# Performance work log

Measured on AMD Instinct MI355X. Metric: run time of the kernel, lower is better.

The kernel has to match this reference:

```python
import jax, jax.numpy as jnp
import numpy as np

B = 8192; L = 68; NPG = L + 1; N = B * NPG
IN = 4; HID = 64; OUT = 7; NL = 8
BN_EPS = 1e-5


def setup_inputs() -> dict:
    key = jax.random.key(0)
    ks = jax.random.split(key, 12)
    # graph topology (same for every graph): ring among L landmarks + master node (idx L)
    # connected to every landmark; directed edges both ways (PyG-style edge_index).
    ring = np.stack([np.arange(L), (np.arange(L) + 1) % L])            # [2, L]
    mast = np.stack([np.arange(L), np.full(L, L)])                     # [2, L]
    und = np.concatenate([ring, mast], axis=1)                         # [2, 2L]
    e = np.concatenate([und, und[::-1]], axis=1)                       # [2, 4L]
    offs = (np.arange(B) * NPG)[:, None, None]
    edge_index = (e[None] + offs).transpose(1, 0, 2).reshape(2, -1)    # [2, B*4L]
    s = 1.0 / np.sqrt(HID)
    return {
        "x": jax.random.normal(ks[0], (N, IN), jnp.float32),
        "edge_index": jnp.asarray(edge_index, jnp.int32),
        "batch": jnp.repeat(jnp.arange(B, dtype=jnp.int32), NPG),
        "master_mask": jnp.tile(jnp.arange(NPG) == L, B),
        "conv_first_W": jax.random.normal(ks[1], (IN, HID), jnp.float32) * 0.5,
        "conv_first_b": jnp.zeros((HID,), jnp.float32),
        "conv_mid_W": jax.random.normal(ks[2], (NL - 2, HID, HID), jnp.float32) * s,
        "conv_mid_b": jnp.zeros((NL - 2, HID), jnp.float32),
        "conv_last_W": jax.random.normal(ks[3], (HID, HID), jnp.float32) * s,
        "conv_last_b": jnp.zeros((HID,), jnp.float32),
        "bn_gamma": jnp.ones((NL - 1, HID), jnp.float32),
        "bn_beta": jnp.zeros((NL - 1, HID), jnp.float32),
        "bn_mean": jax.random.normal(ks[4], (NL - 1, HID), jnp.float32) * 0.1,
        "bn_var": jax.random.uniform(ks[5], (NL - 1, HID), jnp.float32) * 0.5 + 0.5,
        "att_W1": jax.random.normal(ks[6], (HID, HID), jnp.float32) * s,
        "att_b1": jnp.zeros((HID,), jnp.float32),
        "att_W2": jax.random.normal(ks[7], (HID, 1), jnp.float32) * s,
        "att_b2": jnp.zeros((1,), jnp.float32),
        "fc1_W": jax.random.normal(ks[8], (3 * HID, HID), jnp.float32) / np.sqrt(3 * HID),
        "fc1_b": jnp.zeros((HID,), jnp.float32),
        "fc2_W": jax.random.normal(ks[9], (HID, OUT), jnp.float32) * s,
        "fc2_b": jnp.zeros((OUT,), jnp.float32),
    }


def reference(x, edge_index, batch, master_mask,
              conv_first_W, conv_first_b, conv_mid_W, conv_mid_b,
              conv_last_W, conv_last_b, bn_gamma, bn_beta, bn_mean, bn_var,
              att_W1, att_b1, att_W2, att_b2, fc1_W, fc1_b, fc2_W, fc2_b):
    n = x.shape[0]
    src, dst = edge_index[0], edge_index[1]
    # GCN symmetric normalization with self-loops: deg_i = 1 + in-degree
    deg = 1.0 + jax.ops.segment_sum(jnp.ones_like(src, x.dtype), dst, num_segments=n)
    dis = jax.lax.rsqrt(deg)
    enorm = (dis[src] * dis[dst])[:, None]                 # [E,1]
    self_norm = (1.0 / deg)[:, None]                       # [N,1] self-loop coeff

    def gcn(h, W, b):
        h = h @ W                                          # [N,HID]
        agg = jax.ops.segment_sum(h[src] * enorm, dst, num_segments=n)
        return agg + h * self_norm + b

    def bn(h, i):  # eval-mode BatchNorm1d
        return bn_gamma[i] * (h - bn_mean[i]) * jax.lax.rsqrt(bn_var[i] + BN_EPS) + bn_beta[i]

    h = bn(jax.nn.relu(gcn(x, conv_first_W, conv_first_b)), 0)
    for i in range(NL - 2):  # residual GCN blocks
        h = bn(jax.nn.relu(gcn(h, conv_mid_W[i], conv_mid_b[i])), i + 1) + h
    h = jax.nn.relu(gcn(h, conv_last_W, conv_last_b))

    mfl = master_mask.astype(h.dtype)                      # [N]
    mcnt = jax.ops.segment_sum(mfl, batch, num_segments=B)
    master = jax.ops.segment_sum(h * mfl[:, None], batch, num_segments=B) / mcnt[:, None]
    att = jax.nn.sigmoid(jax.nn.relu(master @ att_W1 + att_b1) @ att_W2 + att_b2)
    master = master * att

    rfl = 1.0 - mfl
    rcnt = jax.ops.segment_sum(rfl, batch, num_segments=B)
    x_mean = jax.ops.segment_sum(h * rfl[:, None], batch, num_segments=B) / rcnt[:, None]
    h_masked = jnp.where(master_mask[:, None], -jnp.inf, h)
    x_max = jax.ops.segment_max(h_masked, batch, num_segments=B)

    g = jnp.concatenate([x_mean, x_max, master], axis=1)   # [B, 3*HID]
    return jax.nn.relu(g @ fc1_W + fc1_b) @ fc2_W + fc2_b  # [B, OUT]
```

## Files before the change

kernel.cpp:

```cpp
#include <hip/hip_runtime.h>

typedef float f32x4 __attribute__((ext_vector_type(4)));
typedef short short8 __attribute__((ext_vector_type(8)));
typedef unsigned int u32;
typedef unsigned short u16;

#define CLL 0.25f
#define CML 0.06019292654288460f
#define SELFM 0.014492753623188406f

__device__ __forceinline__ u16 f2bf(float x) {
  u32 b = __float_as_uint(x);
  return (u16)((b + 0x7FFFu + ((b >> 16) & 1u)) >> 16);
}
__device__ __forceinline__ u32 cvtpk(float a, float b) {
  u32 r;
  asm("v_cvt_pk_bf16_f32 %0, %1, %2" : "=v"(r) : "v"(a), "v"(b));
  return r;
}

__global__ void prep(const float* __restrict__ midW, const float* __restrict__ lastW,
                     const float* __restrict__ bng, const float* __restrict__ bnb,
                     const float* __restrict__ bnm, const float* __restrict__ bnv,
                     u16* __restrict__ frag, float* __restrict__ bns) {
  const int t0 = blockIdx.x * blockDim.x + threadIdx.x;
  for (int u = t0; u < 7 * 4 * 2 * 64; u += gridDim.x * blockDim.x) {
    const int lane = u & 63;
    const int t = u >> 6;
    const int ks = t & 1;
    const int nt = (t >> 1) & 3;
    const int l = t >> 3;
    const float* W = (l < 6) ? (midW + l * 4096) : lastW;
    const int col = nt * 16 + (lane & 15);
    const int kb = ks * 32 + (lane >> 4) * 8;
    u16* dst = frag + (size_t)u * 8;
#pragma unroll
    for (int j = 0; j < 8; ++j) dst[j] = f2bf(W[(kb + j) * 64 + col]);
  }
  for (int u = t0; u < 7 * 64; u += gridDim.x * blockDim.x) {
    const int l = u >> 6, f = u & 63;
    const float sc = (float)((double)bng[l * 64 + f] / sqrt((double)bnv[l * 64 + f] + 1e-5));
    bns[l * 128 + f] = sc;
    bns[l * 128 + 64 + f] = bnb[l * 64 + f] - bnm[l * 64 + f] * sc;
  }
}

#define SUM4(V) ((V)[0] + (V)[1] + (V)[2] + (V)[3])
#define MAX4(V) fmaxf(fmaxf((V)[0], (V)[1]), fmaxf((V)[2], (V)[3]))

#define STEP2(MT, TA, TPA, TNA, TB, TPB, TNB, HA, HB, RESID)           \
  {                                                                    \
    const float spA_ = (qg == 3) ? TPA[3] : TA[3];                     \
    const float spB_ = (qg == 3) ? TPB[3] : TB[3];                     \
    const u32 pvP_ = (u32)__shfl((int)cvtpk(spA_, spB_), (lane + 48) & 63, 64); \
    const float snA_ = (qg == 0) ? TNA[0] : TA[0];                     \
    const float snB_ = (qg == 0) ? TNB[0] : TB[0];                     \
    const u32 nvP_ = (u32)__shfl((int)cvtpk(snA_, snB_), (lane + 16) & 63, 64); \
    const float pvA_ = __uint_as_float(pvP_ << 16);                    \
    const float pvB_ = __uint_as_float(pvP_ & 0xffff0000u);            \
    const float nvA_ = __uint_as_float(nvP_ << 16);                    \
    const float nvB_ = __uint_as_float(nvP_ & 0xffff0000u);            \
    const float ta0A_ = ((MT) == 0 && qg == 0) ? tA4[3] : pvA_;        \
    const float ta0B_ = ((MT) == 0 && qg == 0) ? tB4[3] : pvB_;        \
    const float tb3A_ = ((MT) == 4 && qg == 0) ? tA0[0] : nvA_;        \
    const float tb3B_ = ((MT) == 4 && qg == 0) ? tB0[0] : nvB_;        \
    float oA0 = fmaf(CLL, ta0A_ + TA[0] + TA[1], cmtA_);               \
    float oA1 = fmaf(CLL, TA[0] + TA[1] + TA[2], cmtA_);               \
    float oA2 = fmaf(CLL, TA[1] + TA[2] + TA[3], cmtA_);               \
    float oA3 = fmaf(CLL, TA[2] + TA[3] + tb3A_, cmtA_);               \
    float oB0 = fmaf(CLL, ta0B_ + TB[0] + TB[1], cmtB_);               \
    float oB1 = fmaf(CLL, TB[0] + TB[1] + TB[2], cmtB_);               \
    float oB2 = fmaf(CLL, TB[1] + TB[2] + TB[3], cmtB_);               \
    float oB3 = fmaf(CLL, TB[2] + TB[3] + tb3B_, cmtB_);               \
    oA0 = fmaf(fmaxf(oA0, 0.f), scA_, shA_);                           \
    oA1 = fmaf(fmaxf(oA1, 0.f), scA_, shA_);                           \
    oA2 = fmaf(fmaxf(oA2, 0.f), scA_, shA_);                           \
    oA3 = fmaf(fmaxf(oA3, 0.f), scA_, shA_);                           \
    oB0 = fmaf(fmaxf(oB0, 0.f), scB_, shB_);                           \
    oB1 = fmaf(fmaxf(oB1, 0.f), scB_, shB_);                           \
    oB2 = fmaf(fmaxf(oB2, 0.f), scB_, shB_);                           \
    oB3 = fmaf(fmaxf(oB3, 0.f), scB_, shB_);                           \
    if (RESID) {                                                       \
      oA0 += HA[0]; oA1 += HA[1]; oA2 += HA[2]; oA3 += HA[3];          \
      oB0 += HB[0]; oB1 += HB[1]; oB2 += HB[2]; oB3 += HB[3];          \
    }                                                                  \
    HA[0] = oA0; HA[1] = oA1; HA[2] = oA2; HA[3] = oA3;                \
    HB[0] = oB0; HB[1] = oB1; HB[2] = oB2; HB[3] = oB3;                \
  }

#define WPAIR2(HW, MT, H, CQ)                                          \
  {                                                                    \
    const u32 pa = cvtpk(H[0], H[1]);                                  \
    const u32 pb = cvtpk(H[2], H[3]);                                  \
    (HW)[(16 * (MT) + 4 * qg + 0) * 64 + (CQ)] = (u16)pa;              \
    (HW)[(16 * (MT) + 4 * qg + 1) * 64 + ((CQ) ^ 8)] = (u16)(pa >> 16);\
    (HW)[(16 * (MT) + 4 * qg + 2) * 64 + ((CQ) ^ 16)] = (u16)pb;       \
    (HW)[(16 * (MT) + 4 * qg + 3) * 64 + ((CQ) ^ 24)] = (u16)(pb >> 16); \
  }

#define EPILOG2(RESID, WRITE, HBW, BA, BB, SCA, SHA, SCB, SHB)         \
  {                                                                    \
    float SA_ = SUM4(tA0) + SUM4(tA1) + SUM4(tA2) + SUM4(tA3) + SUM4(tA4); \
    float SB_ = SUM4(tB0) + SUM4(tB1) + SUM4(tB2) + SUM4(tB3) + SUM4(tB4); \
    if (qg == 1) { SA_ -= tA4[0]; SB_ -= tB4[0]; }                     \
    SA_ += __shfl_xor(SA_, 16, 64);                                    \
    SA_ += __shfl_xor(SA_, 32, 64);                                    \
    SB_ += __shfl_xor(SB_, 16, 64);                                    \
    SB_ += __shfl_xor(SB_, 32, 64);                                    \
    const u32 pk_ = (u32)__shfl((int)cvtpk(tA4[0], tB4[0]), 16 + p15, 64); \
    const float scA_ = (SCA), shA_ = (SHA), scB_ = (SCB), shB_ = (SHB);\
    const float cmtA_ = fmaf(CML, __uint_as_float(pk_ << 16), (BA));   \
    const float cmtB_ = fmaf(CML, __uint_as_float(pk_ & 0xffff0000u), (BB)); \
    float mvA_ = 0.f, mvB_ = 0.f;                                      \
    if (qg == 1) {                                                     \
      mvA_ = fmaf(fmaxf(fmaf(CML, SA_, fmaf(SELFM, tA4[0], (BA))), 0.f), scA_, shA_); \
      mvB_ = fmaf(fmaxf(fmaf(CML, SB_, fmaf(SELFM, tB4[0], (BB))), 0.f), scB_, shB_); \
      if (RESID) { mvA_ += hA4[0]; mvB_ += hB4[0]; }                   \
    }                                                                  \
    STEP2(0, tA0, tA4, tA1, tB0, tB4, tB1, hA0, hB0, RESID)            \
    STEP2(1, tA1, tA0, tA2, tB1, tB0, tB2, hA1, hB1, RESID)            \
    STEP2(2, tA2, tA1, tA3, tB2, tB1, tB3, hA2, hB2, RESID)            \
    STEP2(3, tA3, tA2, tA4, tB3, tB2, tB4, hA3, hB3, RESID)            \
    STEP2(4, tA4, tA3, tA0, tB4, tB3, tB0, hA4, hB4, RESID)            \
    if (qg == 1) { hA4[0] = mvA_; hB4[0] = mvB_; }                     \
    if (WRITE) {                                                       \
      u16* hw_ = (HBW);                                                \
      WPAIR2(hw_, 0, hA0, cqA) WPAIR2(hw_, 0, hB0, cqB)                \
      WPAIR2(hw_, 1, hA1, cqA) WPAIR2(hw_, 1, hB1, cqB)                \
      WPAIR2(hw_, 2, hA2, cqA) WPAIR2(hw_, 2, hB2, cqB)                \
      WPAIR2(hw_, 3, hA3, cqA) WPAIR2(hw_, 3, hB3, cqB)                \
      if (qg == 0) { WPAIR2(hw_, 4, hA4, cqA) WPAIR2(hw_, 4, hB4, cqB) } \
      else if (qg == 1) {                                              \
        hw_[68 * 64 + (cA ^ 32)] = (u16)cvtpk(mvA_, mvA_);             \
        hw_[68 * 64 + (cB ^ 32)] = (u16)cvtpk(mvB_, mvB_);             \
      }                                                                \
    }                                                                  \
  }

#define MM(A, B, C) __builtin_amdgcn_mfma_f32_16x16x32_bf16(A, B, C, 0, 0, 0)

#define MP3(HR, MT, TA, TB)                                            \
  {                                                                    \
    const short8 a0 = *(const short8*)&(HR)[(MT) * 1024 + ra0];        \
    const short8 a1 = *(const short8*)&(HR)[(MT) * 1024 + ra1];        \
    f32x4 accA = z4, accB = z4;                                        \
    accA = MM(a0, bA0, accA); accA = MM(a1, bA1, accA);                \
    accB = MM(a0, bB0, accB); accB = MM(a1, bB1, accB);                \
    TA = accA; TB = accB;                                              \
  }

__launch_bounds__(128)
__global__ void gcn_fused(
    const float* __restrict__ x,
    const float* __restrict__ cfW, const float* __restrict__ cfb,
    const float* __restrict__ cmb, const float* __restrict__ clb,
    const float* __restrict__ aW1, const float* __restrict__ ab1,
    const float* __restrict__ aW2, const float* __restrict__ ab2,
    const float* __restrict__ f1W, const float* __restrict__ f1b,
    const float* __restrict__ f2W, const float* __restrict__ f2b,
    const u16* __restrict__ frag, const float* __restrict__ bns,
    float* __restrict__ out) {
  __shared__ u16 hb[2][80 * 64];
  __shared__ float xl4[80 * 4];
  __shared__ float mrow[64];
  __shared__ float gv[192];
  __shared__ float part[128];

  const int tid = threadIdx.x;
  const int g = blockIdx.x;
  const int lane = tid & 63;
  const int w = tid >> 6;
  const int p15 = lane & 15;
  const int qg = lane >> 4;
  const int cA = w * 32 + p15;
  const int cB = cA + 16;
  const f32x4 z4 = {0.f, 0.f, 0.f, 0.f};

  const int rsw = (p15 & 7) << 3;
  const int ra0 = (p15 * 64 + qg * 8) ^ rsw;
  const int ra1 = (p15 * 64 + 32 + qg * 8) ^ rsw;
  const int cqA = cA ^ ((qg & 1) << 5);
  const int cqB = cqA ^ 16;

  const u16* f0p = frag + (((size_t)(2 * w) * 2) * 64 + lane) * 8;
  const u16* f1p = frag + (((size_t)(2 * w + 1) * 2) * 64 + lane) * 8;
  short8 bA0 = *(const short8*)f0p;
  short8 bA1 = *(const short8*)(f0p + 512);
  short8 bB0 = *(const short8*)f1p;
  short8 bB1 = *(const short8*)(f1p + 512);

  {
    u32* hz = (u32*)hb;
#pragma unroll
    for (int it = 0; it < 3; ++it) {
      const int i = tid + it * 128;
      if (i < 352) {
        hz[2208 + i] = 0u;
        hz[2560 + 2208 + i] = 0u;
      }
    }
  }
  if (tid < 69)
    *(f32x4*)&xl4[tid * 4] = *(const f32x4*)&x[((size_t)g * 69 + tid) * 4];
  else if (tid < 80)
    *(f32x4*)&xl4[tid * 4] = z4;

  f32x4 tA0, tA1, tA2, tA3, tA4, tB0, tB1, tB2, tB3, tB4;
  f32x4 hA0, hA1, hA2, hA3, hA4, hB0, hB1, hB2, hB3, hB4;

  __syncthreads();

  {
    const float wA0 = cfW[cA], wA1 = cfW[64 + cA], wA2 = cfW[128 + cA], wA3 = cfW[192 + cA];
    const float wB0 = cfW[cB], wB1 = cfW[64 + cB], wB2 = cfW[128 + cB], wB3 = cfW[192 + cB];
#define L0T(MT, TA, TB)                                                \
    { _Pragma("unroll") for (int r = 0; r < 4; ++r) {                  \
        const f32x4 xv = *(const f32x4*)&xl4[(16 * (MT) + 4 * qg + r) * 4]; \
        TA[r] = fmaf(xv[0], wA0, fmaf(xv[1], wA1, fmaf(xv[2], wA2, xv[3] * wA3))); \
        TB[r] = fmaf(xv[0], wB0, fmaf(xv[1], wB1, fmaf(xv[2], wB2, xv[3] * wB3))); } }
    L0T(0, tA0, tB0) L0T(1, tA1, tB1) L0T(2, tA2, tB2) L0T(3, tA3, tB3) L0T(4, tA4, tB4)
#undef L0T
  }
  EPILOG2(false, true, &hb[0][0], cfb[cA], cfb[cB], bns[cA], bns[64 + cA],
          bns[cB], bns[64 + cB])
  __syncthreads();

#pragma unroll 1
  for (int l = 1; l <= 6; ++l) {
    const u16* fA = frag + ((((size_t)l * 4 + 2 * w) * 2) * 64 + lane) * 8;
    const u16* fB = frag + ((((size_t)l * 4 + 2 * w + 1) * 2) * 64 + lane) * 8;
    const short8 nA0 = *(const short8*)fA;
    const short8 nA1 = *(const short8*)(fA + 512);
    const short8 nB0 = *(const short8*)fB;
    const short8 nB1 = *(const short8*)(fB + 512);
    const float biasA = cmb[(l - 1) * 64 + cA];
    const float biasB = cmb[(l - 1) * 64 + cB];
    const float lscA = bns[l * 128 + cA], lshA = bns[l * 128 + 64 + cA];
    const float lscB = bns[l * 128 + cB], lshB = bns[l * 128 + 64 + cB];
    const u16* hr = &hb[(l + 1) & 1][0];
    MP3(hr, 0, tA0, tB0) MP3(hr, 1, tA1, tB1) MP3(hr, 2, tA2, tB2)
    MP3(hr, 3, tA3, tB3) MP3(hr, 4, tA4, tB4)
    bA0 = nA0; bA1 = nA1; bB0 = nB0; bB1 = nB1;
    EPILOG2(true, true, &hb[l & 1][0], biasA, biasB, lscA, lshA, lscB, lshB)
    __syncthreads();
  }

  {
    const u16* hr = &hb[0][0];
    MP3(hr, 0, tA0, tB0) MP3(hr, 1, tA1, tB1) MP3(hr, 2, tA2, tB2)
    MP3(hr, 3, tA3, tB3) MP3(hr, 4, tA4, tB4)
    EPILOG2(false, false, (u16*)nullptr, clb[cA], clb[cB], 1.f, 0.f, 1.f, 0.f)
  }

  {
    float sA = SUM4(hA0) + SUM4(hA1) + SUM4(hA2) + SUM4(hA3);
    float sB = SUM4(hB0) + SUM4(hB1) + SUM4(hB2) + SUM4(hB3);
    float mA = fmaxf(fmaxf(MAX4(hA0), MAX4(hA1)), fmaxf(MAX4(hA2), MAX4(hA3)));
    float mB = fmaxf(fmaxf(MAX4(hB0), MAX4(hB1)), fmaxf(MAX4(hB2), MAX4(hB3)));
    if (qg == 0) {
      sA += SUM4(hA4); mA = fmaxf(mA, MAX4(hA4));
      sB += SUM4(hB4); mB = fmaxf(mB, MAX4(hB4));
    }
    sA += __shfl_xor(sA, 16, 64); sA += __shfl_xor(sA, 32, 64);
    sB += __shfl_xor(sB, 16, 64); sB += __shfl_xor(sB, 32, 64);
    mA = fmaxf(mA, __shfl_xor(mA, 16, 64)); mA = fmaxf(mA, __shfl_xor(mA, 32, 64));
    mB = fmaxf(mB, __shfl_xor(mB, 16, 64)); mB = fmaxf(mB, __shfl_xor(mB, 32, 64));
    if (qg == 0) {
      gv[cA] = sA * (1.f / 68.f);
      gv[64 + cA] = mA;
      gv[cB] = sB * (1.f / 68.f);
      gv[64 + cB] = mB;
    }
    if (qg == 1) { mrow[cA] = hA4[0]; mrow[cB] = hB4[0]; }
  }
  __syncthreads();

  {
    const int f = tid & 63;
    const int kh = tid >> 6;
    float z = 0.f;
#pragma unroll
    for (int k = 0; k < 32; ++k)
      z = fmaf(mrow[kh * 32 + k], aW1[(kh * 32 + k) * 64 + f], z);
    part[tid] = z;
  }
  __syncthreads();
  if (tid < 64) {
    float z = part[tid] + part[64 + tid] + ab1[tid];
    z = fmaxf(z, 0.f);
    float pr = z * aW2[tid];
#pragma unroll
    for (int off = 32; off > 0; off >>= 1) pr += __shfl_xor(pr, off, 64);
    const float att = 1.f / (1.f + expf(-(pr + ab2[0])));
    gv[128 + tid] = mrow[tid] * att;
  }
  __syncthreads();

  {
    const int f = tid & 63;
    const int ih = tid >> 6;
    float a = 0.f;
#pragma unroll
    for (int i = 0; i < 96; ++i)
      a = fmaf(gv[ih * 96 + i], f1W[(ih * 96 + i) * 64 + f], a);
    part[tid] = a;
  }
  __syncthreads();
  if (tid < 64) {
    float a = part[tid] + part[64 + tid] + f1b[tid];
    const float y = fmaxf(a, 0.f);
    float po[7];
#pragma unroll
    for (int o = 0; o < 7; ++o) po[o] = y * f2W[tid * 7 + o];
#pragma unroll
    for (int o = 0; o < 7; ++o)
#pragma unroll
      for (int off = 32; off > 0; off >>= 1) po[o] += __shfl_xor(po[o], off, 64);
    if (tid == 0) {
#pragma unroll
      for (int o = 0; o < 7; ++o) out[(size_t)g * 7 + o] = po[o] + f2b[o];
    }
  }
}

extern "C" void kernel_launch(void* const* d_in, const int* in_sizes, int n_in,
                              void* d_out, int out_size, void* d_ws, size_t ws_size,
                              hipStream_t stream) {
  (void)in_sizes; (void)n_in; (void)ws_size;
  const float* x   = (const float*)d_in[0];
  const float* cfW = (const float*)d_in[4];
  const float* cfb = (const float*)d_in[5];
  const float* cmW = (const float*)d_in[6];
  const float* cmb = (const float*)d_in[7];
  const float* clW = (const float*)d_in[8];
  const float* clb = (const float*)d_in[9];
  const float* bng = (const float*)d_in[10];
  const float* bnb = (const float*)d_in[11];
  const float* bnm = (const float*)d_in[12];
  const float* bnv = (const float*)d_in[13];
  const float* aW1 = (const float*)d_in[14];
  const float* ab1 = (const float*)d_in[15];
  const float* aW2 = (const float*)d_in[16];
  const float* ab2 = (const float*)d_in[17];
  const float* f1W = (const float*)d_in[18];
  const float* f1b = (const float*)d_in[19];
  const float* f2W = (const float*)d_in[20];
  const float* f2b = (const float*)d_in[21];

  u16* frag = (u16*)d_ws;
  float* bns = (float*)((char*)d_ws + 57344);
  const int ngraphs = out_size / 7;

  prep<<<dim3(16), dim3(256), 0, stream>>>(cmW, clW, bng, bnb, bnm, bnv, frag, bns);
  gcn_fused<<<dim3(ngraphs), dim3(128), 0, stream>>>(
      x, cfW, cfb, cmb, clb, aW1, ab1, aW2, ab2, f1W, f1b, f2W, f2b,
      frag, bns, (float*)d_out);
}
```

Before: 157.0 us.

## Map one graph per wavefront, packing four graphs per block without barriers

Previously two wavefronts shared each graph, each computing 32 of the 64 feature columns, and they synchronized with __syncthreads after every layer. Now one wavefront handles a whole graph: it computes all 64 columns in two halves per layer. It reads the A operands into registers first, so the single LDS activation buffer can be overwritten in place. The attention and fc1 head loops run inside the same wave, so block-level barriers and the partial-sum scratch buffer go away. The cost is roughly double the live register state per thread and a serial second half of each layer. That can lower occupancy or cause spills in exchange for less synchronization and fewer blocks.

```diff
diff --git a/kernel.cpp b/kernel.cpp
--- a/kernel.cpp
+++ b/kernel.cpp
@@ -47,6 +47,7 @@
 
 #define SUM4(V) ((V)[0] + (V)[1] + (V)[2] + (V)[3])
 #define MAX4(V) fmaxf(fmaxf((V)[0], (V)[1]), fmaxf((V)[2], (V)[3]))
+#define MM(A, B, C) __builtin_amdgcn_mfma_f32_16x16x32_bf16(A, B, C, 0, 0, 0)
 
 #define STEP2(MT, TA, TPA, TNA, TB, TPB, TNB, HA, HB, RESID)           \
   {                                                                    \
@@ -80,7 +81,7 @@
     oB1 = fmaf(fmaxf(oB1, 0.f), scB_, shB_);                           \
     oB2 = fmaf(fmaxf(oB2, 0.f), scB_, shB_);                           \
     oB3 = fmaf(fmaxf(oB3, 0.f), scB_, shB_);                           \
-    if (RESID) {                                                       \
+    if (RESID) {                                                      \
       oA0 += HA[0]; oA1 += HA[1]; oA2 += HA[2]; oA3 += HA[3];          \
       oB0 += HB[0]; oB1 += HB[1]; oB2 += HB[2]; oB3 += HB[3];          \
     }                                                                  \
@@ -98,15 +99,14 @@
     (HW)[(16 * (MT) + 4 * qg + 3) * 64 + ((CQ) ^ 24)] = (u16)(pb >> 16); \
   }
 
-#define EPILOG2(RESID, WRITE, HBW, BA, BB, SCA, SHA, SCB, SHB)         \
+#define EPILOG2(HA0, HA1, HA2, HA3, HA4, HB0, HB1, HB2, HB3, HB4,      \
+                CQA_, CQB_, CA_, CB_, RESID, WRITE, BA, BB, SCA, SHA, SCB, SHB) \
   {                                                                    \
     float SA_ = SUM4(tA0) + SUM4(tA1) + SUM4(tA2) + SUM4(tA3) + SUM4(tA4); \
     float SB_ = SUM4(tB0) + SUM4(tB1) + SUM4(tB2) + SUM4(tB3) + SUM4(tB4); \
     if (qg == 1) { SA_ -= tA4[0]; SB_ -= tB4[0]; }                     \
-    SA_ += __shfl_xor(SA_, 16, 64);                                    \
-    SA_ += __shfl_xor(SA_, 32, 64);                                    \
-    SB_ += __shfl_xor(SB_, 16, 64);                                    \
-    SB_ += __shfl_xor(SB_, 32, 64);                                    \
+    SA_ += __shfl_xor(SA_, 16, 64); SA_ += __shfl_xor(SA_, 32, 64);    \
+    SB_ += __shfl_xor(SB_, 16, 64); SB_ += __shfl_xor(SB_, 32, 64);    \
     const u32 pk_ = (u32)__shfl((int)cvtpk(tA4[0], tB4[0]), 16 + p15, 64); \
     const float scA_ = (SCA), shA_ = (SHA), scB_ = (SCB), shB_ = (SHB);\
     const float cmtA_ = fmaf(CML, __uint_as_float(pk_ << 16), (BA));   \
@@ -115,41 +115,67 @@
     if (qg == 1) {                                                     \
       mvA_ = fmaf(fmaxf(fmaf(CML, SA_, fmaf(SELFM, tA4[0], (BA))), 0.f), scA_, shA_); \
       mvB_ = fmaf(fmaxf(fmaf(CML, SB_, fmaf(SELFM, tB4[0], (BB))), 0.f), scB_, shB_); \
-      if (RESID) { mvA_ += hA4[0]; mvB_ += hB4[0]; }                   \
+      if (RESID) { mvA_ += HA4[0]; mvB_ += HB4[0]; }                   \
     }                                                                  \
-    STEP2(0, tA0, tA4, tA1, tB0, tB4, tB1, hA0, hB0, RESID)            \
-    STEP2(1, tA1, tA0, tA2, tB1, tB0, tB2, hA1, hB1, RESID)            \
-    STEP2(2, tA2, tA1, tA3, tB2, tB1, tB3, hA2, hB2, RESID)            \
-    STEP2(3, tA3, tA2, tA4, tB3, tB2, tB4, hA3, hB3, RESID)            \
-    STEP2(4, tA4, tA3, tA0, tB4, tB3, tB0, hA4, hB4, RESID)            \
-    if (qg == 1) { hA4[0] = mvA_; hB4[0] = mvB_; }                     \
+    STEP2(0, tA0, tA4, tA1, tB0, tB4, tB1, HA0, HB0, RESID)            \
+    STEP2(1, tA1, tA0, tA2, tB1, tB0, tB2, HA1, HB1, RESID)            \
+    STEP2(2, tA2, tA1, tA3, tB2, tB1, tB3, HA2, HB2, RESID)            \
+    STEP2(3, tA3, tA2, tA4, tB3, tB2, tB4, HA3, HB3, RESID)            \
+    STEP2(4, tA4, tA3, tA0, tB4, tB3, tB0, HA4, HB4, RESID)            \
+    if (qg == 1) { HA4[0] = mvA_; HB4[0] = mvB_; }                     \
     if (WRITE) {                                                       \
-      u16* hw_ = (HBW);                                                \
-      WPAIR2(hw_, 0, hA0, cqA) WPAIR2(hw_, 0, hB0, cqB)                \
-      WPAIR2(hw_, 1, hA1, cqA) WPAIR2(hw_, 1, hB1, cqB)                \
-      WPAIR2(hw_, 2, hA2, cqA) WPAIR2(hw_, 2, hB2, cqB)                \
-      WPAIR2(hw_, 3, hA3, cqA) WPAIR2(hw_, 3, hB3, cqB)                \
-      if (qg == 0) { WPAIR2(hw_, 4, hA4, cqA) WPAIR2(hw_, 4, hB4, cqB) } \
+      WPAIR2(hb, 0, HA0, CQA_) WPAIR2(hb, 0, HB0, CQB_)                \
+      WPAIR2(hb, 1, HA1, CQA_) WPAIR2(hb, 1, HB1, CQB_)                \
+      WPAIR2(hb, 2, HA2, CQA_) WPAIR2(hb, 2, HB2, CQB_)                \
+      WPAIR2(hb, 3, HA3, CQA_) WPAIR2(hb, 3, HB3, CQB_)                \
+      if (qg == 0) { WPAIR2(hb, 4, HA4, CQA_) WPAIR2(hb, 4, HB4, CQB_) } \
       else if (qg == 1) {                                              \
-        hw_[68 * 64 + (cA ^ 32)] = (u16)cvtpk(mvA_, mvA_);             \
-        hw_[68 * 64 + (cB ^ 32)] = (u16)cvtpk(mvB_, mvB_);             \
+        hb[68 * 64 + ((CA_) ^ 32)] = (u16)cvtpk(mvA_, mvA_);           \
+        hb[68 * 64 + ((CB_) ^ 32)] = (u16)cvtpk(mvB_, mvB_);           \
       }                                                                \
     }                                                                  \
   }
 
-#define MM(A, B, C) __builtin_amdgcn_mfma_f32_16x16x32_bf16(A, B, C, 0, 0, 0)
-
-#define MP3(HR, MT, TA, TB)                                            \
-  {                                                                    \
-    const short8 a0 = *(const short8*)&(HR)[(MT) * 1024 + ra0];        \
-    const short8 a1 = *(const short8*)&(HR)[(MT) * 1024 + ra1];        \
-    f32x4 accA = z4, accB = z4;                                        \
-    accA = MM(a0, bA0, accA); accA = MM(a1, bA1, accA);                \
-    accB = MM(a0, bB0, accB); accB = MM(a1, bB1, accB);                \
-    TA = accA; TB = accB;                                              \
-  }
-
-__launch_bounds__(128)
+#define RD_A()                                                         \
+  qa0 = *(const short8*)&hb[0 * 1024 + ra0]; qb0 = *(const short8*)&hb[0 * 1024 + ra1]; \
+  qa1 = *(const short8*)&hb[1 * 1024 + ra0]; qb1 = *(const short8*)&hb[1 * 1024 + ra1]; \
+  qa2 = *(const short8*)&hb[2 * 1024 + ra0]; qb2 = *(const short8*)&hb[2 * 1024 + ra1]; \
+  qa3 = *(const short8*)&hb[3 * 1024 + ra0]; qb3 = *(const short8*)&hb[3 * 1024 + ra1]; \
+  qa4 = *(const short8*)&hb[4 * 1024 + ra0]; qb4 = *(const short8*)&hb[4 * 1024 + ra1];
+
+#define LDB(LF, NT0, NT1)                                              \
+  {                                                                    \
+    const u16* fa_ = frag + (((size_t)(LF) * 4 + (NT0)) * 2 * 64 + lane) * 8; \
+    const u16* fb_ = frag + (((size_t)(LF) * 4 + (NT1)) * 2 * 64 + lane) * 8; \
+    bA0 = *(const short8*)fa_; bA1 = *(const short8*)(fa_ + 512);      \
+    bB0 = *(const short8*)fb_; bB1 = *(const short8*)(fb_ + 512);      \
+  }
+
+#define MPX(QA, QB, TA, TB)                                            \
+  {                                                                    \
+    f32x4 uA_ = z4, uB_ = z4;                                          \
+    uA_ = MM(QA, bA0, uA_); uA_ = MM(QB, bA1, uA_);                    \
+    uB_ = MM(QA, bB0, uB_); uB_ = MM(QB, bB1, uB_);                    \
+    TA = uA_; TB = uB_;                                                \
+  }
+
+#define MFMA_PAIR() \
+  MPX(qa0, qb0, tA0, tB0) MPX(qa1, qb1, tA1, tB1) MPX(qa2, qb2, tA2, tB2) \
+  MPX(qa3, qb3, tA3, tB3) MPX(qa4, qb4, tA4, tB4)
+
+#define RDOUT(H0, H1, H2, H3, H4, C_)                                  \
+  {                                                                    \
+    float s_ = SUM4(H0) + SUM4(H1) + SUM4(H2) + SUM4(H3);              \
+    float m_ = fmaxf(fmaxf(MAX4(H0), MAX4(H1)), fmaxf(MAX4(H2), MAX4(H3))); \
+    if (qg == 0) { s_ += SUM4(H4); m_ = fmaxf(m_, MAX4(H4)); }         \
+    s_ += __shfl_xor(s_, 16, 64); s_ += __shfl_xor(s_, 32, 64);        \
+    m_ = fmaxf(m_, __shfl_xor(m_, 16, 64));                            \
+    m_ = fmaxf(m_, __shfl_xor(m_, 32, 64));                            \
+    if (qg == 0) { gv[C_] = s_ * (1.f / 68.f); gv[64 + C_] = m_; }     \
+    if (qg == 1) mrow[C_] = H4[0];                                     \
+  }
+
+__launch_bounds__(256)
 __global__ void gcn_fused(
     const float* __restrict__ x,
     const float* __restrict__ cfW, const float* __restrict__ cfb,
@@ -159,21 +185,25 @@
     const float* __restrict__ f1W, const float* __restrict__ f1b,
     const float* __restrict__ f2W, const float* __restrict__ f2b,
     const u16* __restrict__ frag, const float* __restrict__ bns,
-    float* __restrict__ out) {
-  __shared__ u16 hb[2][80 * 64];
-  __shared__ float xl4[80 * 4];
-  __shared__ float mrow[64];
-  __shared__ float gv[192];
-  __shared__ float part[128];
-
-  const int tid = threadIdx.x;
-  const int g = blockIdx.x;
-  const int lane = tid & 63;
-  const int w = tid >> 6;
+    float* __restrict__ out, int ngraphs) {
+  __shared__ u16 hbAll[4][80 * 64];
+  __shared__ float xlAll[4][80 * 4];
+  __shared__ float mrowAll[4][64];
+  __shared__ float gvAll[4][192];
+
+  const int lane = threadIdx.x & 63;
+  const int w = threadIdx.x >> 6;
+  const int g = blockIdx.x * 4 + w;
+  if (g >= ngraphs) return;
+
+  u16* hb = hbAll[w];
+  float* xl4 = xlAll[w];
+  float* mrow = mrowAll[w];
+  float* gv = gvAll[w];
+
   const int p15 = lane & 15;
   const int qg = lane >> 4;
-  const int cA = w * 32 + p15;
-  const int cB = cA + 16;
+  const int cA = p15, cB = p15 + 16, cC = p15 + 32, cD = p15 + 48;
   const f32x4 z4 = {0.f, 0.f, 0.f, 0.f};
 
   const int rsw = (p15 & 7) << 3;
@@ -181,142 +211,109 @@
   const int ra1 = (p15 * 64 + 32 + qg * 8) ^ rsw;
   const int cqA = cA ^ ((qg & 1) << 5);
   const int cqB = cqA ^ 16;
-
-  const u16* f0p = frag + (((size_t)(2 * w) * 2) * 64 + lane) * 8;
-  const u16* f1p = frag + (((size_t)(2 * w + 1) * 2) * 64 + lane) * 8;
-  short8 bA0 = *(const short8*)f0p;
-  short8 bA1 = *(const short8*)(f0p + 512);
-  short8 bB0 = *(const short8*)f1p;
-  short8 bB1 = *(const short8*)(f1p + 512);
-
-  {
-    u32* hz = (u32*)hb;
-#pragma unroll
-    for (int it = 0; it < 3; ++it) {
-      const int i = tid + it * 128;
-      if (i < 352) {
-        hz[2208 + i] = 0u;
-        hz[2560 + 2208 + i] = 0u;
-      }
-    }
-  }
-  if (tid < 69)
-    *(f32x4*)&xl4[tid * 4] = *(const f32x4*)&x[((size_t)g * 69 + tid) * 4];
-  else if (tid < 80)
-    *(f32x4*)&xl4[tid * 4] = z4;
+  const int cqC = cqA ^ 32;
+  const int cqD = cqA ^ 48;
+
+  for (int i = lane; i < 352; i += 64) ((u32*)hb)[2208 + i] = 0u;
+  *(f32x4*)&xl4[lane * 4] = *(const f32x4*)&x[((size_t)g * 69 + lane) * 4];
+  if (lane < 5)
+    *(f32x4*)&xl4[(64 + lane) * 4] = *(const f32x4*)&x[((size_t)g * 69 + 64 + lane) * 4];
+  else if (lane < 16)
+    *(f32x4*)&xl4[(64 + lane) * 4] = z4;
 
   f32x4 tA0, tA1, tA2, tA3, tA4, tB0, tB1, tB2, tB3, tB4;
   f32x4 hA0, hA1, hA2, hA3, hA4, hB0, hB1, hB2, hB3, hB4;
-
-  __syncthreads();
-
-  {
-    const float wA0 = cfW[cA], wA1 = cfW[64 + cA], wA2 = cfW[128 + cA], wA3 = cfW[192 + cA];
-    const float wB0 = cfW[cB], wB1 = cfW[64 + cB], wB2 = cfW[128 + cB], wB3 = cfW[192 + cB];
-#define L0T(MT, TA, TB)                                                \
-    { _Pragma("unroll") for (int r = 0; r < 4; ++r) {                  \
-        const f32x4 xv = *(const f32x4*)&xl4[(16 * (MT) + 4 * qg + r) * 4]; \
-        TA[r] = fmaf(xv[0], wA0, fmaf(xv[1], wA1, fmaf(xv[2], wA2, xv[3] * wA3))); \
-        TB[r] = fmaf(xv[0], wB0, fmaf(xv[1], wB1, fmaf(xv[2], wB2, xv[3] * wB3))); } }
-    L0T(0, tA0, tB0) L0T(1, tA1, tB1) L0T(2, tA2, tB2) L0T(3, tA3, tB3) L0T(4, tA4, tB4)
+  f32x4 hC0, hC1, hC2, hC3, hC4, hD0, hD1, hD2, hD3, hD4;
+  short8 qa0, qa1, qa2, qa3, qa4, qb0, qb1, qb2, qb3, qb4;
+  short8 bA0, bA1, bB0, bB1;
+
+#define L0T(MT, TA, TB, W0A, W1A, W2A, W3A, W0B, W1B, W2B, W3B)        \
+  { _Pragma("unroll") for (int r = 0; r < 4; ++r) {                    \
+      const f32x4 xv = *(const f32x4*)&xl4[(16 * (MT) + 4 * qg + r) * 4]; \
+      TA[r] = fmaf(xv[0], W0A, fmaf(xv[1], W1A, fmaf(xv[2], W2A, xv[3] * W3A))); \
+      TB[r] = fmaf(xv[0], W0B, fmaf(xv[1], W1B, fmaf(xv[2], W2B, xv[3] * W3B))); } }
+  {
+    const float a0 = cfW[cA], a1 = cfW[64 + cA], a2 = cfW[128 + cA], a3 = cfW[192 + cA];
+    const float b0 = cfW[cB], b1 = cfW[64 + cB], b2 = cfW[128 + cB], b3 = cfW[192 + cB];
+    L0T(0, tA0, tB0, a0, a1, a2, a3, b0, b1, b2, b3)
+    L0T(1, tA1, tB1, a0, a1, a2, a3, b0, b1, b2, b3)
+    L0T(2, tA2, tB2, a0, a1, a2, a3, b0, b1, b2, b3)
+    L0T(3, tA3, tB3, a0, a1, a2, a3, b0, b1, b2, b3)
+    L0T(4, tA4, tB4, a0, a1, a2, a3, b0, b1, b2, b3)
+    EPILOG2(hA0, hA1, hA2, hA3, hA4, hB0, hB1, hB2, hB3, hB4, cqA, cqB, cA, cB,
+            false, true, cfb[cA], cfb[cB], bns[cA], bns[64 + cA], bns[cB], bns[64 + cB])
+  }
+  {
+    const float a0 = cfW[cC], a1 = cfW[64 + cC], a2 = cfW[128 + cC], a3 = cfW[192 + cC];
+    const float b0 = cfW[cD], b1 = cfW[64 + cD], b2 = cfW[128 + cD], b3 = cfW[192 + cD];
+    L0T(0, tA0, tB0, a0, a1, a2, a3, b0, b1, b2, b3)
+    L0T(1, tA1, tB1, a0, a1, a2, a3, b0, b1, b2, b3)
+    L0T(2, tA2, tB2, a0, a1, a2, a3, b0, b1, b2, b3)
+    L0T(3, tA3, tB3, a0, a1, a2, a3, b0, b1, b2, b3)
+    L0T(4, tA4, tB4, a0, a1, a2, a3, b0, b1, b2, b3)
+    EPILOG2(hC0, hC1, hC2, hC3, hC4, hD0, hD1, hD2, hD3, hD4, cqC, cqD, cC, cD,
+            false, true, cfb[cC], cfb[cD], bns[cC], bns[64 + cC], bns[cD], bns[64 + cD])
+  }
 #undef L0T
-  }
-  EPILOG2(false, true, &hb[0][0], cfb[cA], cfb[cB], bns[cA], bns[64 + cA],
-          bns[cB], bns[64 + cB])
-  __syncthreads();
 
 #pragma unroll 1
   for (int l = 1; l <= 6; ++l) {
-    const u16* fA = frag + ((((size_t)l * 4 + 2 * w) * 2) * 64 + lane) * 8;
-    const u16* fB = frag + ((((size_t)l * 4 + 2 * w + 1) * 2) * 64 + lane) * 8;
-    const short8 nA0 = *(const short8*)fA;
-    const short8 nA1 = *(const short8*)(fA + 512);
-    const short8 nB0 = *(const short8*)fB;
-    const short8 nB1 = *(const short8*)(fB + 512);
-    const float biasA = cmb[(l - 1) * 64 + cA];
-    const float biasB = cmb[(l - 1) * 64 + cB];
-    const float lscA = bns[l * 128 + cA], lshA = bns[l * 128 + 64 + cA];
-    const float lscB = bns[l * 128 + cB], lshB = bns[l * 128 + 64 + cB];
-    const u16* hr = &hb[(l + 1) & 1][0];
-    MP3(hr, 0, tA0, tB0) MP3(hr, 1, tA1, tB1) MP3(hr, 2, tA2, tB2)
-    MP3(hr, 3, tA3, tB3) MP3(hr, 4, tA4, tB4)
-    bA0 = nA0; bA1 = nA1; bB0 = nB0; bB1 = nB1;
-    EPILOG2(true, true, &hb[l & 1][0], biasA, biasB, lscA, lshA, lscB, lshB)
-    __syncthreads();
-  }
-
-  {
-    const u16* hr = &hb[0][0];
-    MP3(hr, 0, tA0, tB0) MP3(hr, 1, tA1, tB1) MP3(hr, 2, tA2, tB2)
-    MP3(hr, 3, tA3, tB3) MP3(hr, 4, tA4, tB4)
-    EPILOG2(false, false, (u16*)nullptr, clb[cA], clb[cB], 1.f, 0.f, 1.f, 0.f)
-  }
-
-  {
-    float sA = SUM4(hA0) + SUM4(hA1) + SUM4(hA2) + SUM4(hA3);
-    float sB = SUM4(hB0) + SUM4(hB1) + SUM4(hB2) + SUM4(hB3);
-    float mA = fmaxf(fmaxf(MAX4(hA0), MAX4(hA1)), fmaxf(MAX4(hA2), MAX4(hA3)));
-    float mB = fmaxf(fmaxf(MAX4(hB0), MAX4(hB1)), fmaxf(MAX4(hB2), MAX4(hB3)));
-    if (qg == 0) {
-      sA += SUM4(hA4); mA = fmaxf(mA, MAX4(hA4));
-      sB += SUM4(hB4); mB = fmaxf(mB, MAX4(hB4));
-    }
-    sA += __shfl_xor(sA, 16, 64); sA += __shfl_xor(sA, 32, 64);
-    sB += __shfl_xor(sB, 16, 64); sB += __shfl_xor(sB, 32, 64);
-    mA = fmaxf(mA, __shfl_xor(mA, 16, 64)); mA = fmaxf(mA, __shfl_xor(mA, 32, 64));
-    mB = fmaxf(mB, __shfl_xor(mB, 16, 64)); mB = fmaxf(mB, __shfl_xor(mB, 32, 64));
-    if (qg == 0) {
-      gv[cA] = sA * (1.f / 68.f);
-      gv[64 + cA] = mA;
-      gv[cB] = sB * (1.f / 68.f);
-      gv[64 + cB] = mB;
-    }
-    if (qg == 1) { mrow[cA] = hA4[0]; mrow[cB] = hB4[0]; }
-  }
-  __syncthreads();
-
-  {
-    const int f = tid & 63;
-    const int kh = tid >> 6;
+    RD_A()
+    LDB(l - 1, 0, 1)
+    MFMA_PAIR()
+    EPILOG2(hA0, hA1, hA2, hA3, hA4, hB0, hB1, hB2, hB3, hB4, cqA, cqB, cA, cB,
+            true, true, cmb[(l - 1) * 64 + cA], cmb[(l - 1) * 64 + cB],
+            bns[l * 128 + cA], bns[l * 128 + 64 + cA],
+            bns[l * 128 + cB], bns[l * 128 + 64 + cB])
+    LDB(l - 1, 2, 3)
+    MFMA_PAIR()
+    EPILOG2(hC0, hC1, hC2, hC3, hC4, hD0, hD1, hD2, hD3, hD4, cqC, cqD, cC, cD,
+            true, true, cmb[(l - 1) * 64 + cC], cmb[(l - 1) * 64 + cD],
+            bns[l * 128 + cC], bns[l * 128 + 64 + cC],
+            bns[l * 128 + cD], bns[l * 128 + 64 + cD])
+  }
+
+  {
+    RD_A()
+    LDB(6, 0, 1)
+    MFMA_PAIR()
+    EPILOG2(hA0, hA1, hA2, hA3, hA4, hB0, hB1, hB2, hB3, hB4, cqA, cqB, cA, cB,
+            false, false, clb[cA], clb[cB], 1.f, 0.f, 1.f, 0.f)
+    LDB(6, 2, 3)
+    MFMA_PAIR()
+    EPILOG2(hC0, hC1, hC2, hC3, hC4, hD0, hD1, hD2, hD3, hD4, cqC, cqD, cC, cD,
+            false, false, clb[cC], clb[cD], 1.f, 0.f, 1.f, 0.f)
+  }
+
+  RDOUT(hA0, hA1, hA2, hA3, hA4, cA)
+  RDOUT(hB0, hB1, hB2, hB3, hB4, cB)
+  RDOUT(hC0, hC1, hC2, hC3, hC4, cC)
+  RDOUT(hD0, hD1, hD2, hD3, hD4, cD)
+
+  {
     float z = 0.f;
-#pragma unroll
-    for (int k = 0; k < 32; ++k)
-      z = fmaf(mrow[kh * 32 + k], aW1[(kh * 32 + k) * 64 + f], z);
-    part[tid] = z;
-  }
-  __syncthreads();
-  if (tid < 64) {
-    float z = part[tid] + part[64 + tid] + ab1[tid];
-    z = fmaxf(z, 0.f);
-    float pr = z * aW2[tid];
+#pragma unroll 4
+    for (int k = 0; k < 64; ++k) z = fmaf(mrow[k], aW1[k * 64 + lane], z);
+    z = fmaxf(z + ab1[lane], 0.f);
+    float pr = z * aW2[lane];
 #pragma unroll
     for (int off = 32; off > 0; off >>= 1) pr += __shfl_xor(pr, off, 64);
     const float att = 1.f / (1.f + expf(-(pr + ab2[0])));
-    gv[128 + tid] = mrow[tid] * att;
-  }
-  __syncthreads();
-
-  {
-    const int f = tid & 63;
-    const int ih = tid >> 6;
-    float a = 0.f;
-#pragma unroll
-    for (int i = 0; i < 96; ++i)
-      a = fmaf(gv[ih * 96 + i], f1W[(ih * 96 + i) * 64 + f], a);
-    part[tid] = a;
-  }
-  __syncthreads();
-  if (tid < 64) {
-    float a = part[tid] + part[64 + tid] + f1b[tid];
+    gv[128 + lane] = mrow[lane] * att;
+  }
+  {
+    float a = f1b[lane];
+#pragma unroll 4
+    for (int i = 0; i < 192; ++i) a = fmaf(gv[i], f1W[i * 64 + lane], a);
     const float y = fmaxf(a, 0.f);
     float po[7];
 #pragma unroll
-    for (int o = 0; o < 7; ++o) po[o] = y * f2W[tid * 7 + o];
+    for (int o = 0; o < 7; ++o) po[o] = y * f2W[lane * 7 + o];
 #pragma unroll
     for (int o = 0; o < 7; ++o)
 #pragma unroll
       for (int off = 32; off > 0; off >>= 1) po[o] += __shfl_xor(po[o], off, 64);
-    if (tid == 0) {
+    if (lane == 0) {
 #pragma unroll
       for (int o = 0; o < 7; ++o) out[(size_t)g * 7 + o] = po[o] + f2b[o];
     }
@@ -350,9 +347,10 @@
   u16* frag = (u16*)d_ws;
   float* bns = (float*)((char*)d_ws + 57344);
   const int ngraphs = out_size / 7;
+  const int nblocks = (ngraphs + 3) / 4;
 
   prep<<<dim3(16), dim3(256), 0, stream>>>(cmW, clW, bng, bnb, bnm, bnv, frag, bns);
-  gcn_fused<<<dim3(ngraphs), dim3(128), 0, stream>>>(
+  gcn_fused<<<dim3(nblocks), dim3(256), 0, stream>>>(
       x, cfW, cfb, cmb, clb, aW1, ab1, aW2, ab2, f1W, f1b, f2W, f2b,
-      frag, bns, (float*)d_out);
-}
+      frag, bns, (float*)d_out, ngraphs);
+}
```

Result: slower. 265.1 us (+68.8%).
